# Performance work log

Measured on AMD Instinct MI355X. Metric: run time of the kernel, lower is better.

Reference implementation:

```python
import jax, jax.numpy as jnp
import numpy as np
import math

EPS_LN = 1e-5
EPS_Q = 1e-5


def _layernorm(x):
    # LayerNorm without affine (elementwise_affine=False), biased variance
    mu = jnp.mean(x, axis=-1, keepdims=True)
    var = jnp.var(x, axis=-1, keepdims=True)
    return (x - mu) * jax.lax.rsqrt(var + EPS_LN)


def _quantize_activations(x):
    # per-row 8-bit absmax quantization
    eta = jnp.maximum(jnp.max(jnp.abs(x), axis=-1, keepdims=True), EPS_Q)
    x_q = jnp.clip(jnp.round(x * (127.0 / eta)), -128.0, 127.0)
    return x_q, eta / 127.0


def _quantize_weights(w):
    # absmean ternary quantization
    gamma = jnp.maximum(jnp.mean(jnp.abs(w)), EPS_Q)
    w_q = jnp.round(jnp.clip(w / gamma, -1.0, 1.0))
    return w_q, gamma


def setup_inputs() -> dict:
    key = jax.random.key(0)
    k1, k2 = jax.random.split(key, 2)
    B, S, IN, OUT = 2, 4096, 2048, 8192
    x = jax.random.normal(k1, (B, S, IN), dtype=jnp.float32)
    # kaiming_uniform_(a=sqrt(5)) -> U(-1/sqrt(fan_in), 1/sqrt(fan_in))
    bound = 1.0 / math.sqrt(IN)
    weight = jax.random.uniform(k2, (OUT, IN), dtype=jnp.float32, minval=-bound, maxval=bound)
    bias = jnp.zeros((OUT,), dtype=jnp.float32)
    return {"x": x, "weight": weight, "bias": bias}


def reference(x, weight, bias):
    x_norm = _layernorm(x)
    x_q, x_scale = _quantize_activations(x_norm)      # [B,S,K], [B,S,1]
    w_q, w_scale = _quantize_weights(weight)           # [N,K], scalar
    # int8 GEMM emulated exactly in fp32 (values are small integers, exact)
    out_i = jnp.einsum('bsk,nk->bsn', x_q, w_q)        # int32-equivalent accum
    out = out_i * (w_scale * x_scale) + bias
    return out
```

## Files before the change

kernel.cpp:

```cpp
#include <hip/hip_runtime.h>
#include <stdint.h>

typedef int v4i __attribute__((ext_vector_type(4)));

#define M_DIM 8192
#define N_DIM 8192
#define K_DIM 2048
#define RISKY_TAU 1e-4f
#define BUCKET_CAP 1024

#define ASYNC16(g, l) __builtin_amdgcn_global_load_lds(                        \
    (const __attribute__((address_space(1))) void*)(uintptr_t)(g),             \
    (__attribute__((address_space(3))) void*)(uint32_t)(uintptr_t)(l), 16, 0, 0)

__global__ __launch_bounds__(256) void abssum_stage1(const float* __restrict__ w,
                                                     float* __restrict__ s1) {
  int b = blockIdx.x * 256 + threadIdx.x;
  const float* p = w + (size_t)b * 128;
  float r[8];
#pragma unroll
  for (int j = 0; j < 8; j++) r[j] = fabsf(p[j]);
  for (int i = 8; i < 128; i += 8) {
#pragma unroll
    for (int j = 0; j < 8; j++) r[j] += fabsf(p[i + j]);
  }
  s1[b] = ((r[0] + r[1]) + (r[2] + r[3])) + ((r[4] + r[5]) + (r[6] + r[7]));
}

__global__ __launch_bounds__(256) void abssum_stage2(const float* __restrict__ s1,
                                                     float* __restrict__ s2) {
  int t = blockIdx.x * 256 + threadIdx.x;
  float v[32];
#pragma unroll
  for (int i = 0; i < 32; i++) v[i] = s1[t * 32 + i];
#pragma unroll
  for (int s = 1; s < 32; s *= 2) {
#pragma unroll
    for (int i = 0; i < 32; i += 2 * s) v[i] += v[i + s];
  }
  s2[t] = v[0];
}

__global__ __launch_bounds__(256) void gamma_stage3(const float* __restrict__ s2,
                                                    float* __restrict__ gp) {
  int t = threadIdx.x;
  float v[16];
#pragma unroll
  for (int i = 0; i < 16; i++) v[i] = s2[t * 16 + i];
#pragma unroll
  for (int s = 1; s < 16; s *= 2) {
#pragma unroll
    for (int i = 0; i < 16; i += 2 * s) v[i] += v[i + s];
  }
  __shared__ float sm[256];
  sm[t] = v[0];
  for (int s = 1; s < 256; s *= 2) {
    __syncthreads();
    if ((t & (2 * s - 1)) == 0) sm[t] += sm[t + s];
  }
  __syncthreads();
  if (t == 0) {
    float g = sm[0] * 0x1p-24f;
    gp[0] = fmaxf(g, 1e-5f);
  }
}

__global__ void zero_counts(int* __restrict__ counts) {
  counts[threadIdx.x] = 0;
}

__global__ __launch_bounds__(256) void wq_kernel(const float4* __restrict__ w4,
                                                 const float* __restrict__ gp,
                                                 int* __restrict__ wq,
                                                 int* __restrict__ counts,
                                                 int* __restrict__ buckets) {
  int i = blockIdx.x * 256 + threadIdx.x;
  float g = gp[0];
  float4 v = w4[i];
  float e[4] = {v.x, v.y, v.z, v.w};
  int q[4];
#pragma unroll
  for (int c = 0; c < 4; c++) {
    q[c] = (int)rintf(fminf(fmaxf(e[c] / g, -1.0f), 1.0f));
    float t = fabsf(e[c]) / g;
    if (fabsf(t - 0.5f) < RISKY_TAU) {
      int flat = i * 4 + c;
      int n = flat >> 11;
      int k = flat & 2047;
      int sgn_neg = (e[c] < 0.0f) ? 1 : 0;
      int sbit = (q[c] == 0) ? sgn_neg : (1 - sgn_neg);
      int b = n >> 7;
      int idx = atomicAdd(&counts[b], 1);
      if (idx < BUCKET_CAP)
        buckets[b * BUCKET_CAP + idx] = k | (n << 11) | (sbit << 24);
    }
  }
  wq[i] = (q[0] & 0xFF) | ((q[1] & 0xFF) << 8) | ((q[2] & 0xFF) << 16) | ((q[3] & 0xFF) << 24);
}

__global__ __launch_bounds__(256) void lnq_kernel(const float* __restrict__ x,
                                                  const float* __restrict__ gp,
                                                  int8_t* __restrict__ xq,
                                                  float* __restrict__ scales) {
  const int row = blockIdx.x;
  const int t = threadIdx.x;
  const float4* xr = (const float4*)(x + (size_t)row * K_DIM);
  float4 a = xr[t];
  float4 b = xr[t + 256];
  double v[8] = {a.x, a.y, a.z, a.w, b.x, b.y, b.z, b.w};
  double s = 0.0, ss = 0.0;
#pragma unroll
  for (int i = 0; i < 8; i++) { s += v[i]; ss += v[i] * v[i]; }
  __shared__ double sm1[256], sm2[256];
  sm1[t] = s; sm2[t] = ss;
  __syncthreads();
  for (int off = 128; off > 0; off >>= 1) {
    if (t < off) { sm1[t] += sm1[t + off]; sm2[t] += sm2[t + off]; }
    __syncthreads();
  }
  double mu = sm1[0] * (1.0 / 2048.0);
  double var = sm2[0] * (1.0 / 2048.0) - mu * mu;
  double inv = 1.0 / sqrt(var + 1e-5);
  __syncthreads();
  double mx = 0.0;
#pragma unroll
  for (int i = 0; i < 8; i++) {
    v[i] = (v[i] - mu) * inv;
    double av = fabs(v[i]);
    if (av > mx) mx = av;
  }
  sm1[t] = mx;
  __syncthreads();
  for (int off = 128; off > 0; off >>= 1) {
    if (t < off) sm1[t] = fmax(sm1[t], sm1[t + off]);
    __syncthreads();
  }
  double eta = fmax(sm1[0], 1e-5);
  double r = 127.0 / eta;
  int q[8];
#pragma unroll
  for (int i = 0; i < 8; i++) {
    double qq = rint(v[i] * r);
    qq = fmin(fmax(qq, -128.0), 127.0);
    q[i] = (int)qq;
  }
  int p0 = (q[0] & 0xFF) | ((q[1] & 0xFF) << 8) | ((q[2] & 0xFF) << 16) | ((q[3] & 0xFF) << 24);
  int p1 = (q[4] & 0xFF) | ((q[5] & 0xFF) << 8) | ((q[6] & 0xFF) << 16) | ((q[7] & 0xFF) << 24);
  int* orow = (int*)(xq + (size_t)row * K_DIM);
  orow[t] = p0;
  orow[t + 256] = p1;
  if (t == 0) scales[row] = (float)((double)gp[0] * eta * (1.0 / 127.0));
}

__global__ __launch_bounds__(256) void gemm_i8_kernel(const int8_t* __restrict__ A,
                                                      const int8_t* __restrict__ B,
                                                      const float* __restrict__ scales,
                                                      const float* __restrict__ bias,
                                                      const int* __restrict__ counts,
                                                      const int* __restrict__ buckets,
                                                      float* __restrict__ C) {
  __shared__ alignas(16) int8_t lds[2 * 128 * 64];
  const int tid = threadIdx.x;
  const int wave = tid >> 6;
  const int lane = tid & 63;
  const int brow = blockIdx.y * 128;
  const int bcol = blockIdx.x * 128;

  const int rA0 = (wave * 2 + 0) * 16 + (lane >> 2);
  const int rA1 = (wave * 2 + 1) * 16 + (lane >> 2);
  const int c16 = lane & 3;
  const int cA0 = ((c16 ^ ((rA0 >> 1) & 3)) << 4);
  const int cA1 = ((c16 ^ ((rA1 >> 1) & 3)) << 4);
  const int8_t* gA0 = A + (size_t)(brow + rA0) * K_DIM + cA0;
  const int8_t* gA1 = A + (size_t)(brow + rA1) * K_DIM + cA1;
  const int8_t* gB0 = B + (size_t)(bcol + rA0) * K_DIM + cA0;
  const int8_t* gB1 = B + (size_t)(bcol + rA1) * K_DIM + cA1;
  int8_t* lA0 = lds + (wave * 2 + 0) * 1024;
  int8_t* lA1 = lds + (wave * 2 + 1) * 1024;
  int8_t* lB0 = lds + 8192 + (wave * 2 + 0) * 1024;
  int8_t* lB1 = lds + 8192 + (wave * 2 + 1) * 1024;

  const int wr = wave >> 1, wc = wave & 1;
  int aoff[4], boff[4];
#pragma unroll
  for (int i = 0; i < 4; i++) {
    int lr = wr * 64 + i * 16 + (lane & 15);
    aoff[i] = lr * 64 + ((((lane >> 4) ^ ((lr >> 1) & 3))) << 4);
    int lc = wc * 64 + i * 16 + (lane & 15);
    boff[i] = 8192 + lc * 64 + ((((lane >> 4) ^ ((lc >> 1) & 3))) << 4);
  }

  v4i acc[4][4];
  const v4i vzero = {0, 0, 0, 0};
#pragma unroll
  for (int i = 0; i < 4; i++)
#pragma unroll
    for (int j = 0; j < 4; j++) acc[i][j] = vzero;

  for (int kt = 0; kt < K_DIM; kt += 64) {
    ASYNC16(gA0 + kt, lA0);
    ASYNC16(gA1 + kt, lA1);
    ASYNC16(gB0 + kt, lB0);
    ASYNC16(gB1 + kt, lB1);
    __syncthreads();
    v4i af[4], bf[4];
#pragma unroll
    for (int i = 0; i < 4; i++) af[i] = *(const v4i*)(lds + aoff[i]);
#pragma unroll
    for (int j = 0; j < 4; j++) bf[j] = *(const v4i*)(lds + boff[j]);
#pragma unroll
    for (int i = 0; i < 4; i++)
#pragma unroll
      for (int j = 0; j < 4; j++)
        acc[i][j] = __builtin_amdgcn_mfma_i32_16x16x64_i8(af[i], bf[j], acc[i][j], 0, 0, 0);
    __syncthreads();
  }

#pragma unroll
  for (int i = 0; i < 4; i++)
#pragma unroll
    for (int j = 0; j < 4; j++) acc[i][j] = acc[i][j] + acc[i][j];

  const int crow0 = brow + wr * 64;
  const int ccol0 = bcol + wc * 64;

#define CORR(J)                                                                \
  {                                                                            \
    _Pragma("unroll") for (int i = 0; i < 4; i++) {                            \
      _Pragma("unroll") for (int r = 0; r < 4; r++) {                          \
        int grow = crow0 + i * 16 + ((lane >> 4) << 2) + r;                    \
        int xv = (int)A[(size_t)grow * K_DIM + k];                             \
        acc[i][J][r] += sv * xv;                                               \
      }                                                                        \
    }                                                                          \
  }

  {
    int bkt = bcol >> 7;
    int cnt = counts[bkt];
    if (cnt > BUCKET_CAP) cnt = BUCKET_CAP;
    const int* bk = buckets + bkt * BUCKET_CAP;
    for (int e = 0; e < cnt; ++e) {
      int word = bk[e];
      int k = word & 2047;
      int n = (word >> 11) & 8191;
      int sv = ((word >> 24) & 1) ? -1 : 1;
      int lc = n - bcol;
      if (((lc >> 6) & 1) == wc && (lc & 15) == (lane & 15)) {
        int j = (lc >> 4) & 3;
        switch (j) {
          case 0: CORR(0); break;
          case 1: CORR(1); break;
          case 2: CORR(2); break;
          case 3: CORR(3); break;
        }
      }
    }
  }
#undef CORR

#pragma unroll
  for (int i = 0; i < 4; i++) {
#pragma unroll
    for (int r = 0; r < 4; r++) {
      int grow = crow0 + i * 16 + ((lane >> 4) << 2) + r;
      float sc = scales[grow] * 0.5f;
      float* crow = C + (size_t)grow * N_DIM;
#pragma unroll
      for (int j = 0; j < 4; j++) {
        int gcol = ccol0 + j * 16 + (lane & 15);
        crow[gcol] = (float)acc[i][j][r] * sc + bias[gcol];
      }
    }
  }
}

extern "C" void kernel_launch(void* const* d_in, const int* in_sizes, int n_in,
                              void* d_out, int out_size, void* d_ws, size_t ws_size,
                              hipStream_t stream) {
  const float* x = (const float*)d_in[0];
  const float* w = (const float*)d_in[1];
  const float* bias = (const float*)d_in[2];
  float* out = (float*)d_out;

  char* ws = (char*)d_ws;
  float* s1 = (float*)(ws);
  float* s2 = (float*)(ws + 0x100000);
  float* gamma_f = (float*)(ws + 0x110000);
  float* scales = (float*)(ws + 0x120000);
  int* counts = (int*)(ws + 0x130000);
  int* buckets = (int*)(ws + 0x131000);
  int8_t* Aq = (int8_t*)(ws + 0x200000);
  int8_t* Wq = (int8_t*)(ws + 0x200000 + (size_t)M_DIM * K_DIM);

  abssum_stage1<<<512, 256, 0, stream>>>(w, s1);
  abssum_stage2<<<16, 256, 0, stream>>>(s1, s2);
  gamma_stage3<<<1, 256, 0, stream>>>(s2, gamma_f);
  zero_counts<<<1, 64, 0, stream>>>(counts);
  wq_kernel<<<(N_DIM * K_DIM / 4 + 255) / 256, 256, 0, stream>>>(
      (const float4*)w, gamma_f, (int*)Wq, counts, buckets);
  lnq_kernel<<<M_DIM, 256, 0, stream>>>(x, gamma_f, Aq, scales);
  dim3 grid(N_DIM / 128, M_DIM / 128);
  gemm_i8_kernel<<<grid, 256, 0, stream>>>(Aq, Wq, scales, bias, counts, buckets, out);
}
```

Before: 314.1 us.

## Restructure int8 GEMM into 256x256 tiles with triple-buffered async LDS pipeline

Replaces the 128x128, 4-wave GEMM with a 256x256, 8-wave block that uses a three-stage LDS ring of async global-to-LDS loads. Each K step is split into two MFMA phases interleaved with the next stage's loads. The change also adds s_setprio around MFMAs and a swizzled 1D block index for L2 locality. The aim is to hide global load latency and raise data reuse per block. In exchange it uses 96KB of LDS and more accumulator registers, and the bucket correction lookup now maps columns differently.

```diff
diff --git a/kernel.cpp b/kernel.cpp
--- a/kernel.cpp
+++ b/kernel.cpp
@@ -152,102 +152,143 @@
   if (t == 0) scales[row] = (float)((double)gp[0] * eta * (1.0 / 127.0));
 }
 
-__global__ __launch_bounds__(256) void gemm_i8_kernel(const int8_t* __restrict__ A,
-                                                      const int8_t* __restrict__ B,
-                                                      const float* __restrict__ scales,
-                                                      const float* __restrict__ bias,
-                                                      const int* __restrict__ counts,
-                                                      const int* __restrict__ buckets,
-                                                      float* __restrict__ C) {
-  __shared__ alignas(16) int8_t lds[2 * 128 * 64];
+__global__ __launch_bounds__(512, 2) void gemm_i8_kernel(const int8_t* __restrict__ A,
+                                                         const int8_t* __restrict__ B,
+                                                         const float* __restrict__ scales,
+                                                         const float* __restrict__ bias,
+                                                         const int* __restrict__ counts,
+                                                         const int* __restrict__ buckets,
+                                                         float* __restrict__ C) {
+  __shared__ alignas(16) int8_t lds[3 * 32768];
   const int tid = threadIdx.x;
-  const int wave = tid >> 6;
+  const int w = tid >> 6;
   const int lane = tid & 63;
-  const int brow = blockIdx.y * 128;
-  const int bcol = blockIdx.x * 128;
-
-  const int rA0 = (wave * 2 + 0) * 16 + (lane >> 2);
-  const int rA1 = (wave * 2 + 1) * 16 + (lane >> 2);
-  const int c16 = lane & 3;
-  const int cA0 = ((c16 ^ ((rA0 >> 1) & 3)) << 4);
-  const int cA1 = ((c16 ^ ((rA1 >> 1) & 3)) << 4);
-  const int8_t* gA0 = A + (size_t)(brow + rA0) * K_DIM + cA0;
-  const int8_t* gA1 = A + (size_t)(brow + rA1) * K_DIM + cA1;
-  const int8_t* gB0 = B + (size_t)(bcol + rA0) * K_DIM + cA0;
-  const int8_t* gB1 = B + (size_t)(bcol + rA1) * K_DIM + cA1;
-  int8_t* lA0 = lds + (wave * 2 + 0) * 1024;
-  int8_t* lA1 = lds + (wave * 2 + 1) * 1024;
-  int8_t* lB0 = lds + 8192 + (wave * 2 + 0) * 1024;
-  int8_t* lB1 = lds + 8192 + (wave * 2 + 1) * 1024;
-
-  const int wr = wave >> 1, wc = wave & 1;
-  int aoff[4], boff[4];
-#pragma unroll
-  for (int i = 0; i < 4; i++) {
-    int lr = wr * 64 + i * 16 + (lane & 15);
-    aoff[i] = lr * 64 + ((((lane >> 4) ^ ((lr >> 1) & 3))) << 4);
-    int lc = wc * 64 + i * 16 + (lane & 15);
-    boff[i] = 8192 + lc * 64 + ((((lane >> 4) ^ ((lc >> 1) & 3))) << 4);
-  }
-
-  v4i acc[4][4];
+
+  const int bid = blockIdx.x;
+  const int swz = (bid & 7) * 128 + (bid >> 3);
+  const int brow = (swz >> 5) * 256;
+  const int bcol = (swz & 31) * 256;
+
+  const int wr = w >> 2;
+  const int wc = w & 3;
+
+  const int srccol = ((lane & 3) ^ ((lane >> 3) & 3)) << 4;
+  const int rq = w * 16 + (lane >> 2);
+  const int8_t* gA0 = A + (size_t)(brow + rq) * K_DIM + srccol;
+  const int8_t* gA1 = A + (size_t)(brow + 128 + rq) * K_DIM + srccol;
+  const int8_t* gB0 = B + (size_t)(bcol + rq) * K_DIM + srccol;
+  const int8_t* gB1 = B + (size_t)(bcol + 128 + rq) * K_DIM + srccol;
+  const int stA = (w * 16) * 64 + lane * 16;
+  const int stA1 = stA + 8192;
+
+  int aoff[8], boff[4];
+#pragma unroll
+  for (int m = 0; m < 8; m++) {
+    int r = wr * 128 + m * 16 + (lane & 15);
+    aoff[m] = r * 64 + ((((lane >> 4) ^ ((r >> 1) & 3))) << 4);
+  }
+#pragma unroll
+  for (int n = 0; n < 4; n++) {
+    int r = wc * 64 + n * 16 + (lane & 15);
+    boff[n] = 16384 + r * 64 + ((((lane >> 4) ^ ((r >> 1) & 3))) << 4);
+  }
+
+  v4i acc[8][4];
   const v4i vzero = {0, 0, 0, 0};
 #pragma unroll
-  for (int i = 0; i < 4; i++)
-#pragma unroll
-    for (int j = 0; j < 4; j++) acc[i][j] = vzero;
-
-  for (int kt = 0; kt < K_DIM; kt += 64) {
-    ASYNC16(gA0 + kt, lA0);
-    ASYNC16(gA1 + kt, lA1);
-    ASYNC16(gB0 + kt, lB0);
-    ASYNC16(gB1 + kt, lB1);
-    __syncthreads();
-    v4i af[4], bf[4];
-#pragma unroll
-    for (int i = 0; i < 4; i++) af[i] = *(const v4i*)(lds + aoff[i]);
-#pragma unroll
-    for (int j = 0; j < 4; j++) bf[j] = *(const v4i*)(lds + boff[j]);
-#pragma unroll
-    for (int i = 0; i < 4; i++)
-#pragma unroll
-      for (int j = 0; j < 4; j++)
-        acc[i][j] = __builtin_amdgcn_mfma_i32_16x16x64_i8(af[i], bf[j], acc[i][j], 0, 0, 0);
-    __syncthreads();
-  }
-
-#pragma unroll
-  for (int i = 0; i < 4; i++)
-#pragma unroll
-    for (int j = 0; j < 4; j++) acc[i][j] = acc[i][j] + acc[i][j];
-
-  const int crow0 = brow + wr * 64;
+  for (int m = 0; m < 8; m++)
+#pragma unroll
+    for (int n = 0; n < 4; n++) acc[m][n] = vzero;
+
+  ASYNC16(gA0, lds + stA);
+  ASYNC16(gB0, lds + 16384 + stA);
+  ASYNC16(gA1, lds + stA1);
+  ASYNC16(gB1, lds + 16384 + stA1);
+  ASYNC16(gA0 + 64, lds + 32768 + stA);
+  ASYNC16(gB0 + 64, lds + 32768 + 16384 + stA);
+  ASYNC16(gA1 + 64, lds + 32768 + stA1);
+  ASYNC16(gB1 + 64, lds + 32768 + 16384 + stA1);
+  asm volatile("s_waitcnt vmcnt(4)" ::: "memory");
+  __builtin_amdgcn_s_barrier();
+
+  int rbase = 0;
+  int sbase = 2 * 32768;
+  for (int t = 0; t < 32; ++t) {
+    const bool st = (t < 30);
+    const int kt = (t + 2) * 64;
+    v4i bf[4], af[4];
+#pragma unroll
+    for (int n = 0; n < 4; n++) bf[n] = *(const v4i*)(lds + rbase + boff[n]);
+#pragma unroll
+    for (int m = 0; m < 4; m++) af[m] = *(const v4i*)(lds + rbase + aoff[m]);
+    if (st) {
+      ASYNC16(gA0 + kt, lds + sbase + stA);
+      ASYNC16(gB0 + kt, lds + sbase + 16384 + stA);
+    }
+    __builtin_amdgcn_s_barrier();
+    __builtin_amdgcn_s_setprio(1);
+#pragma unroll
+    for (int m = 0; m < 4; m++)
+#pragma unroll
+      for (int n = 0; n < 4; n++)
+        acc[m][n] = __builtin_amdgcn_mfma_i32_16x16x64_i8(af[m], bf[n], acc[m][n], 0, 0, 0);
+    __builtin_amdgcn_s_setprio(0);
+    __builtin_amdgcn_s_barrier();
+#pragma unroll
+    for (int m = 0; m < 4; m++) af[m] = *(const v4i*)(lds + rbase + aoff[4 + m]);
+    if (st) {
+      ASYNC16(gA1 + kt, lds + sbase + stA1);
+      ASYNC16(gB1 + kt, lds + sbase + 16384 + stA1);
+    }
+    __builtin_amdgcn_s_barrier();
+    __builtin_amdgcn_s_setprio(1);
+#pragma unroll
+    for (int m = 0; m < 4; m++)
+#pragma unroll
+      for (int n = 0; n < 4; n++)
+        acc[4 + m][n] = __builtin_amdgcn_mfma_i32_16x16x64_i8(af[m], bf[n], acc[4 + m][n], 0, 0, 0);
+    __builtin_amdgcn_s_setprio(0);
+    if (t < 30) {
+      asm volatile("s_waitcnt vmcnt(4)" ::: "memory");
+    } else if (t == 30) {
+      asm volatile("s_waitcnt vmcnt(0)" ::: "memory");
+    }
+    __builtin_amdgcn_s_barrier();
+    rbase = (rbase == 2 * 32768) ? 0 : rbase + 32768;
+    sbase = (sbase == 2 * 32768) ? 0 : sbase + 32768;
+  }
+
+#pragma unroll
+  for (int m = 0; m < 8; m++)
+#pragma unroll
+    for (int n = 0; n < 4; n++) acc[m][n] = acc[m][n] + acc[m][n];
+
+  const int crow0 = brow + wr * 128;
   const int ccol0 = bcol + wc * 64;
 
 #define CORR(J)                                                                \
   {                                                                            \
-    _Pragma("unroll") for (int i = 0; i < 4; i++) {                            \
+    _Pragma("unroll") for (int m = 0; m < 8; m++) {                            \
       _Pragma("unroll") for (int r = 0; r < 4; r++) {                          \
-        int grow = crow0 + i * 16 + ((lane >> 4) << 2) + r;                    \
+        int grow = crow0 + m * 16 + ((lane >> 4) << 2) + r;                    \
         int xv = (int)A[(size_t)grow * K_DIM + k];                             \
-        acc[i][J][r] += sv * xv;                                               \
+        acc[m][J][r] += sv * xv;                                               \
       }                                                                        \
     }                                                                          \
   }
 
   {
-    int bkt = bcol >> 7;
+    int bkt = (bcol + wc * 64) >> 7;
     int cnt = counts[bkt];
     if (cnt > BUCKET_CAP) cnt = BUCKET_CAP;
     const int* bk = buckets + bkt * BUCKET_CAP;
     for (int e = 0; e < cnt; ++e) {
       int word = bk[e];
       int k = word & 2047;
-      int n = (word >> 11) & 8191;
+      int nc = (word >> 11) & 8191;
       int sv = ((word >> 24) & 1) ? -1 : 1;
-      int lc = n - bcol;
-      if (((lc >> 6) & 1) == wc && (lc & 15) == (lane & 15)) {
-        int j = (lc >> 4) & 3;
+      if (((nc >> 6) & 1) == (wc & 1) && (nc & 15) == (lane & 15)) {
+        int j = (nc >> 4) & 3;
         switch (j) {
           case 0: CORR(0); break;
           case 1: CORR(1); break;
@@ -260,16 +301,16 @@
 #undef CORR
 
 #pragma unroll
-  for (int i = 0; i < 4; i++) {
+  for (int m = 0; m < 8; m++) {
 #pragma unroll
     for (int r = 0; r < 4; r++) {
-      int grow = crow0 + i * 16 + ((lane >> 4) << 2) + r;
+      int grow = crow0 + m * 16 + ((lane >> 4) << 2) + r;
       float sc = scales[grow] * 0.5f;
       float* crow = C + (size_t)grow * N_DIM;
 #pragma unroll
-      for (int j = 0; j < 4; j++) {
-        int gcol = ccol0 + j * 16 + (lane & 15);
-        crow[gcol] = (float)acc[i][j][r] * sc + bias[gcol];
+      for (int n = 0; n < 4; n++) {
+        int gcol = ccol0 + n * 16 + (lane & 15);
+        crow[gcol] = (float)acc[m][n][r] * sc + bias[gcol];
       }
     }
   }
@@ -300,6 +341,5 @@
   wq_kernel<<<(N_DIM * K_DIM / 4 + 255) / 256, 256, 0, stream>>>(
       (const float4*)w, gamma_f, (int*)Wq, counts, buckets);
   lnq_kernel<<<M_DIM, 256, 0, stream>>>(x, gamma_f, Aq, scales);
-  dim3 grid(N_DIM / 128, M_DIM / 128);
-  gemm_i8_kernel<<<grid, 256, 0, stream>>>(Aq, Wq, scales, bias, counts, buckets, out);
-}
+  gemm_i8_kernel<<<1024, 512, 0, stream>>>(Aq, Wq, scales, bias, counts, buckets, out);
+}
```

New measurement: 808.9 us. 2.58x slower.

## Triple-buffer LDS in int8 GEMM with async prefetch two tiles ahead

Applied to the files above, without the earlier changes.

The GEMM main loop previously loaded each K-tile into LDS and waited on it immediately, with two barriers per iteration and no overlap between global loads and MFMA work. It now uses three LDS slots, prefetches tiles two iterations ahead, and waits on the load counter with a single barrier per iteration. MFMA issue is also wrapped in s_setprio. This raises LDS use to 48KB per block and adds a 3-blocks-per-CU launch-bounds hint, which may limit occupancy and register budget.

```diff
diff --git a/kernel.cpp b/kernel.cpp
--- a/kernel.cpp
+++ b/kernel.cpp
@@ -8,6 +8,7 @@
 #define K_DIM 2048
 #define RISKY_TAU 1e-4f
 #define BUCKET_CAP 1024
+#define SLOT 16384
 
 #define ASYNC16(g, l) __builtin_amdgcn_global_load_lds(                        \
     (const __attribute__((address_space(1))) void*)(uintptr_t)(g),             \
@@ -152,14 +153,14 @@
   if (t == 0) scales[row] = (float)((double)gp[0] * eta * (1.0 / 127.0));
 }
 
-__global__ __launch_bounds__(256) void gemm_i8_kernel(const int8_t* __restrict__ A,
-                                                      const int8_t* __restrict__ B,
-                                                      const float* __restrict__ scales,
-                                                      const float* __restrict__ bias,
-                                                      const int* __restrict__ counts,
-                                                      const int* __restrict__ buckets,
-                                                      float* __restrict__ C) {
-  __shared__ alignas(16) int8_t lds[2 * 128 * 64];
+__global__ __launch_bounds__(256, 3) void gemm_i8_kernel(const int8_t* __restrict__ A,
+                                                         const int8_t* __restrict__ B,
+                                                         const float* __restrict__ scales,
+                                                         const float* __restrict__ bias,
+                                                         const int* __restrict__ counts,
+                                                         const int* __restrict__ buckets,
+                                                         float* __restrict__ C) {
+  __shared__ alignas(16) int8_t lds[3 * SLOT];
   const int tid = threadIdx.x;
   const int wave = tid >> 6;
   const int lane = tid & 63;
@@ -175,10 +176,10 @@
   const int8_t* gA1 = A + (size_t)(brow + rA1) * K_DIM + cA1;
   const int8_t* gB0 = B + (size_t)(bcol + rA0) * K_DIM + cA0;
   const int8_t* gB1 = B + (size_t)(bcol + rA1) * K_DIM + cA1;
-  int8_t* lA0 = lds + (wave * 2 + 0) * 1024;
-  int8_t* lA1 = lds + (wave * 2 + 1) * 1024;
-  int8_t* lB0 = lds + 8192 + (wave * 2 + 0) * 1024;
-  int8_t* lB1 = lds + 8192 + (wave * 2 + 1) * 1024;
+  const int dA0 = (wave * 2 + 0) * 1024;
+  const int dA1 = (wave * 2 + 1) * 1024;
+  const int dB0 = 8192 + (wave * 2 + 0) * 1024;
+  const int dB1 = 8192 + (wave * 2 + 1) * 1024;
 
   const int wr = wave >> 1, wc = wave & 1;
   int aoff[4], boff[4];
@@ -197,23 +198,43 @@
 #pragma unroll
     for (int j = 0; j < 4; j++) acc[i][j] = vzero;
 
-  for (int kt = 0; kt < K_DIM; kt += 64) {
-    ASYNC16(gA0 + kt, lA0);
-    ASYNC16(gA1 + kt, lA1);
-    ASYNC16(gB0 + kt, lB0);
-    ASYNC16(gB1 + kt, lB1);
-    __syncthreads();
+  ASYNC16(gA0, lds + dA0);
+  ASYNC16(gA1, lds + dA1);
+  ASYNC16(gB0, lds + dB0);
+  ASYNC16(gB1, lds + dB1);
+  ASYNC16(gA0 + 64, lds + SLOT + dA0);
+  ASYNC16(gA1 + 64, lds + SLOT + dA1);
+  ASYNC16(gB0 + 64, lds + SLOT + dB0);
+  ASYNC16(gB1 + 64, lds + SLOT + dB1);
+
+  int rbase = 0;
+  int sbase = 2 * SLOT;
+  for (int t = 0; t < 32; ++t) {
+    if (t < 31) asm volatile("s_waitcnt vmcnt(4)" ::: "memory");
+    else        asm volatile("s_waitcnt vmcnt(0)" ::: "memory");
+    __builtin_amdgcn_s_barrier();
+    asm volatile("" ::: "memory");
+    if (t < 30) {
+      const int kt = (t + 2) * 64;
+      ASYNC16(gA0 + kt, lds + sbase + dA0);
+      ASYNC16(gA1 + kt, lds + sbase + dA1);
+      ASYNC16(gB0 + kt, lds + sbase + dB0);
+      ASYNC16(gB1 + kt, lds + sbase + dB1);
+    }
     v4i af[4], bf[4];
 #pragma unroll
-    for (int i = 0; i < 4; i++) af[i] = *(const v4i*)(lds + aoff[i]);
-#pragma unroll
-    for (int j = 0; j < 4; j++) bf[j] = *(const v4i*)(lds + boff[j]);
+    for (int i = 0; i < 4; i++) af[i] = *(const v4i*)(lds + rbase + aoff[i]);
+#pragma unroll
+    for (int j = 0; j < 4; j++) bf[j] = *(const v4i*)(lds + rbase + boff[j]);
+    __builtin_amdgcn_s_setprio(1);
 #pragma unroll
     for (int i = 0; i < 4; i++)
 #pragma unroll
       for (int j = 0; j < 4; j++)
         acc[i][j] = __builtin_amdgcn_mfma_i32_16x16x64_i8(af[i], bf[j], acc[i][j], 0, 0, 0);
-    __syncthreads();
+    __builtin_amdgcn_s_setprio(0);
+    rbase = (rbase == 2 * SLOT) ? 0 : rbase + SLOT;
+    sbase = (sbase == 2 * SLOT) ? 0 : sbase + SLOT;
   }
 
 #pragma unroll
```

New measurement: 548.1 us. 74.5% more time.
